# Kernel optimization log

Hardware: AMD Instinct MI355X
Metric: run time of the kernel (lower is better)

Reference implementation:

```python
import jax, jax.numpy as jnp
import numpy as np

N = 40000      # num nodes
E = 640000     # num edges (avg degree 16)
D = 128        # hidden_size
L = 2          # num_gcn


def setup_inputs() -> dict:
    key = jax.random.key(0)
    k1, k2, k3, k4, k5, k6 = jax.random.split(key, 6)
    h = jax.random.normal(k1, (N, D), dtype=jnp.float32)
    edge_src = jax.random.randint(k2, (E,), 0, N, dtype=jnp.int32)
    edge_dst = jax.random.randint(k3, (E,), 0, N, dtype=jnp.int32)
    w_self = jax.random.uniform(k4, (E,), dtype=jnp.float32)
    w_ppi = jax.random.uniform(k5, (E,), dtype=jnp.float32)
    # Xavier-uniform linear weights, zero bias (matches reset_parameters)
    limit = float(np.sqrt(6.0 / (D + D)))
    W = jax.random.uniform(k6, (L, D, D), dtype=jnp.float32, minval=-limit, maxval=limit)
    b = jnp.zeros((L, D), dtype=jnp.float32)
    return {"h": h, "edge_src": edge_src, "edge_dst": edge_dst,
            "w_self": w_self, "w_ppi": w_ppi, "W": W, "b": b}


def _agg(h, src, dst, w):
    # edge-weighted SpMM: sum over incoming edges of w_e * h[src_e]
    msgs = h[src] * w[:, None]                       # [E, D]
    return jax.ops.segment_sum(msgs, dst, num_segments=N)  # [N, D]


def reference(h, edge_src, edge_dst, w_self, w_ppi, W, b):
    for l in range(L):
        res = _agg(h, edge_src, edge_dst, w_self)        # residual aggregation
        ppi = _agg(h, edge_src, edge_dst, w_ppi)         # ppi aggregation
        # NodeUpdate: dropout(relu(linear(ppi))) + res  (dropout=0 -> identity)
        h = jax.nn.relu(ppi @ W[l].T + b[l]) + res
    return h
```

## Files before the change

kernel.cpp:

```cpp
#include <hip/hip_runtime.h>

#define D 128
#define TILE 16
#define CAP 64

typedef short bf16x8 __attribute__((ext_vector_type(8)));
typedef float f32x4  __attribute__((ext_vector_type(4)));
typedef float f32x2  __attribute__((ext_vector_type(2)));

static __device__ __forceinline__ unsigned f2bf(float x) {
    unsigned u = __float_as_uint(x);
    return (u + 0x7FFFu + ((u >> 16) & 1u)) >> 16;
}
static __device__ __forceinline__ float blo(unsigned v) { return __uint_as_float(v << 16); }
static __device__ __forceinline__ float bhi(unsigned v) { return __uint_as_float(v & 0xFFFF0000u); }

__global__ __launch_bounds__(256) void cvt2z_kernel(const float4* __restrict__ a,
                                                    uint2* __restrict__ oa, int n4a,
                                                    const float4* __restrict__ bsrc,
                                                    uint2* __restrict__ ob, int n4b,
                                                    int4* __restrict__ zbuf, int nz4) {
    int i = blockIdx.x * 256 + threadIdx.x;
    if (i < n4a) {
        float4 v = a[i];
        uint2 o;
        o.x = f2bf(v.x) | (f2bf(v.y) << 16);
        o.y = f2bf(v.z) | (f2bf(v.w) << 16);
        oa[i] = o;
    }
    int j = i - n4a;
    if (j >= 0 && j < n4b) {
        float4 v = bsrc[j];
        uint2 o;
        o.x = f2bf(v.x) | (f2bf(v.y) << 16);
        o.y = f2bf(v.z) | (f2bf(v.w) << 16);
        ob[j] = o;
    }
    int k = j - n4b;
    if (k >= 0 && k < nz4) zbuf[k] = make_int4(0, 0, 0, 0);
}

__global__ __launch_bounds__(256) void build_kernel(const int* __restrict__ src,
                                                    const int* __restrict__ dst,
                                                    const float* __restrict__ wself,
                                                    const float* __restrict__ wppi,
                                                    int* __restrict__ cnt,
                                                    uint2* __restrict__ edges, int E) {
    int i = blockIdx.x * 256 + threadIdx.x;
    if (i < E) {
        int d = dst[i];
        int r = atomicAdd(&cnt[d], 1);
        if (r < CAP) {
            uint2 e;
            e.x = (unsigned)src[i];
            e.y = f2bf(wself[i]) | (f2bf(wppi[i]) << 16);
            edges[(d << 6) + r] = e;
        }
    }
}

__global__ __launch_bounds__(512, 6) void layer_kernel(const unsigned short* __restrict__ h16,
                                                       const int* __restrict__ cnt,
                                                       const uint2* __restrict__ edges,
                                                       const unsigned short* __restrict__ Wb,
                                                       const float* __restrict__ bias,
                                                       float* __restrict__ out,
                                                       unsigned short* __restrict__ out16,
                                                       int n) {
    __shared__ unsigned short ppi_lds[TILE][136];
    __shared__ float          res_lds[TILE][132];
    int t = threadIdx.x;
    int w = t >> 6, lane = t & 63;
    int tile = blockIdx.x;
    int q  = lane >> 4;
    int c8 = lane & 15;

    #pragma unroll
    for (int sub = 0; sub < 2; ++sub) {
        int nd   = sub * 8 + w;
        int node = tile * TILE + nd;
        int beg = node << 6;
        int end = beg + cnt[node];
        f32x2 ra[4] = {{0.f,0.f},{0.f,0.f},{0.f,0.f},{0.f,0.f}};
        f32x2 pa[4] = {{0.f,0.f},{0.f,0.f},{0.f,0.f},{0.f,0.f}};
        if (beg < end) {
            int e = beg;
            for (; e + 16 <= end; e += 16) {
                uint2 er[4];
                #pragma unroll
                for (int j = 0; j < 4; ++j) er[j] = edges[e + 4 * j + q];
                uint4 hv[4];
                #pragma unroll
                for (int j = 0; j < 4; ++j)
                    hv[j] = *(const uint4*)(h16 + (size_t)er[j].x * D + c8 * 8);
                #pragma unroll
                for (int j = 0; j < 4; ++j) {
                    float a = blo(er[j].y), b = bhi(er[j].y);
                    f32x2 av = {a, a}, bv = {b, b};
                    f32x2 h01 = {blo(hv[j].x), bhi(hv[j].x)};
                    f32x2 h23 = {blo(hv[j].y), bhi(hv[j].y)};
                    f32x2 h45 = {blo(hv[j].z), bhi(hv[j].z)};
                    f32x2 h67 = {blo(hv[j].w), bhi(hv[j].w)};
                    ra[0] = __builtin_elementwise_fma(av, h01, ra[0]);
                    ra[1] = __builtin_elementwise_fma(av, h23, ra[1]);
                    ra[2] = __builtin_elementwise_fma(av, h45, ra[2]);
                    ra[3] = __builtin_elementwise_fma(av, h67, ra[3]);
                    pa[0] = __builtin_elementwise_fma(bv, h01, pa[0]);
                    pa[1] = __builtin_elementwise_fma(bv, h23, pa[1]);
                    pa[2] = __builtin_elementwise_fma(bv, h45, pa[2]);
                    pa[3] = __builtin_elementwise_fma(bv, h67, pa[3]);
                }
            }
            if (e < end) {
                uint2 er[4];
                float sc[4];
                #pragma unroll
                for (int j = 0; j < 4; ++j) {
                    int idx = e + 4 * j + q;
                    bool act = idx < end;
                    er[j] = edges[act ? idx : beg];
                    sc[j] = act ? 1.f : 0.f;
                }
                uint4 hv[4];
                #pragma unroll
                for (int j = 0; j < 4; ++j)
                    hv[j] = *(const uint4*)(h16 + (size_t)er[j].x * D + c8 * 8);
                #pragma unroll
                for (int j = 0; j < 4; ++j) {
                    float a = blo(er[j].y) * sc[j], b = bhi(er[j].y) * sc[j];
                    f32x2 av = {a, a}, bv = {b, b};
                    f32x2 h01 = {blo(hv[j].x), bhi(hv[j].x)};
                    f32x2 h23 = {blo(hv[j].y), bhi(hv[j].y)};
                    f32x2 h45 = {blo(hv[j].z), bhi(hv[j].z)};
                    f32x2 h67 = {blo(hv[j].w), bhi(hv[j].w)};
                    ra[0] = __builtin_elementwise_fma(av, h01, ra[0]);
                    ra[1] = __builtin_elementwise_fma(av, h23, ra[1]);
                    ra[2] = __builtin_elementwise_fma(av, h45, ra[2]);
                    ra[3] = __builtin_elementwise_fma(av, h67, ra[3]);
                    pa[0] = __builtin_elementwise_fma(bv, h01, pa[0]);
                    pa[1] = __builtin_elementwise_fma(bv, h23, pa[1]);
                    pa[2] = __builtin_elementwise_fma(bv, h45, pa[2]);
                    pa[3] = __builtin_elementwise_fma(bv, h67, pa[3]);
                }
            }
        }
        float r[8] = {ra[0].x, ra[0].y, ra[1].x, ra[1].y, ra[2].x, ra[2].y, ra[3].x, ra[3].y};
        float p[8] = {pa[0].x, pa[0].y, pa[1].x, pa[1].y, pa[2].x, pa[2].y, pa[3].x, pa[3].y};
        #pragma unroll
        for (int i = 0; i < 8; ++i) {
            r[i] += __shfl_xor(r[i], 16, 64);
            r[i] += __shfl_xor(r[i], 32, 64);
            p[i] += __shfl_xor(p[i], 16, 64);
            p[i] += __shfl_xor(p[i], 32, 64);
        }
        if (q == 0) {
            *(float4*)&res_lds[nd][c8 * 8]     = make_float4(r[0], r[1], r[2], r[3]);
            *(float4*)&res_lds[nd][c8 * 8 + 4] = make_float4(r[4], r[5], r[6], r[7]);
            uint4 o;
            o.x = f2bf(p[0]) | (f2bf(p[1]) << 16);
            o.y = f2bf(p[2]) | (f2bf(p[3]) << 16);
            o.z = f2bf(p[4]) | (f2bf(p[5]) << 16);
            o.w = f2bf(p[6]) | (f2bf(p[7]) << 16);
            *(uint4*)&ppi_lds[nd][c8 * 8] = o;
        }
    }
    __syncthreads();

    {
        int m16 = lane & 15, quad = lane >> 4;
        bf16x8 a[4];
        const unsigned short* arow = &ppi_lds[m16][quad * 8];
        #pragma unroll
        for (int kt = 0; kt < 4; ++kt) a[kt] = *(const bf16x8*)(arow + kt * 32);

        const unsigned short* brow = Wb + (size_t)(w * 16 + m16) * D + quad * 8;
        bf16x8 bfr[4];
        #pragma unroll
        for (int kt = 0; kt < 4; ++kt) bfr[kt] = *(const bf16x8*)(brow + kt * 32);

        f32x4 acc = {0.f, 0.f, 0.f, 0.f};
        #pragma unroll
        for (int kt = 0; kt < 4; ++kt)
            acc = __builtin_amdgcn_mfma_f32_16x16x32_bf16(a[kt], bfr[kt], acc, 0, 0, 0);

        int o = w * 16 + m16;
        float bb = bias[o];
        #pragma unroll
        for (int r = 0; r < 4; ++r) {
            int nd = quad * 4 + r;
            float v = fmaxf(acc[r] + bb, 0.f) + res_lds[nd][o];
            size_t gi = (size_t)(tile * TILE + nd) * D + o;
            if (out)   out[gi] = v;
            if (out16) out16[gi] = (unsigned short)f2bf(v);
        }
    }
}

extern "C" void kernel_launch(void* const* d_in, const int* in_sizes, int n_in,
                              void* d_out, int out_size, void* d_ws, size_t ws_size,
                              hipStream_t stream) {
    const float* h0    = (const float*)d_in[0];
    const int*   esrc  = (const int*)d_in[1];
    const int*   edst  = (const int*)d_in[2];
    const float* wself = (const float*)d_in[3];
    const float* wppi  = (const float*)d_in[4];
    const float* W     = (const float*)d_in[5];
    const float* b     = (const float*)d_in[6];
    float*       out   = (float*)d_out;

    const int N = in_sizes[0] / D;
    const int E = in_sizes[1];
    const int L = in_sizes[5] / (D * D);

    char* ws = (char*)d_ws;
    unsigned short* h16a  = (unsigned short*)ws; ws += (size_t)N * D * 2;
    unsigned short* h16b  = (unsigned short*)ws; ws += (size_t)N * D * 2;
    uint2*          edges = (uint2*)ws;          ws += (size_t)N * CAP * 8;
    unsigned short* Wb    = (unsigned short*)ws; ws += (size_t)L * D * D * 2;
    int* cnt = (int*)ws;  ws += (size_t)N * 4;

    int n4h = N * D / 4;
    int n4w = L * D * D / 4;
    int nz4 = N / 4;
    int tot = n4h + n4w + nz4;
    cvt2z_kernel<<<(tot + 255) / 256, 256, 0, stream>>>(
        (const float4*)h0, (uint2*)h16a, n4h,
        (const float4*)W, (uint2*)Wb, n4w,
        (int4*)cnt, nz4);

    int eb = (E + 255) / 256;
    build_kernel<<<eb, 256, 0, stream>>>(esrc, edst, wself, wppi, cnt, edges, E);

    int ntiles = N / TILE;
    layer_kernel<<<ntiles, 512, 0, stream>>>(h16a, cnt, edges, Wb, b,
                                             (L > 1) ? nullptr : out,
                                             (L > 1) ? h16b : nullptr, N);
    for (int l = 1; l < L; ++l) {
        bool last = (l + 1 == L);
        layer_kernel<<<ntiles, 512, 0, stream>>>(h16b, cnt, edges,
                                                 Wb + (size_t)l * D * D, b + (size_t)l * D,
                                                 last ? out : nullptr,
                                                 last ? nullptr : h16a, N);
        unsigned short* tmp = h16a; h16a = h16b; h16b = tmp;
    }
}
```

Baseline: 191.3 us.

## Prefetch edge lists for both nodes and hoist weight loads before aggregation

Loads the first 32 edge records for both nodes of each wave up front, and also the MFMA weight fragments and bias before the gather phase. Each node's first 16 or 32 feature rows are then gathered in one batch, with a loop only for the remaining edges. The aim is more memory-level parallelism and hiding edge-load latency behind feature gathers. In exchange it raises register pressure (launch bounds occupancy hint lowered from 6 to 4) and adds clamping of source indices to the node range.

```diff
diff --git a/kernel.cpp b/kernel.cpp
--- a/kernel.cpp
+++ b/kernel.cpp
@@ -59,7 +59,77 @@
     }
 }
 
-__global__ __launch_bounds__(512, 6) void layer_kernel(const unsigned short* __restrict__ h16,
+static __device__ __forceinline__ void edge_fma(uint2 er, uint4 hv, float sc,
+                                                f32x2 (&ra)[4], f32x2 (&pa)[4]) {
+    float a = blo(er.y) * sc, b = bhi(er.y) * sc;
+    f32x2 av = {a, a}, bv = {b, b};
+    f32x2 h01 = {blo(hv.x), bhi(hv.x)};
+    f32x2 h23 = {blo(hv.y), bhi(hv.y)};
+    f32x2 h45 = {blo(hv.z), bhi(hv.z)};
+    f32x2 h67 = {blo(hv.w), bhi(hv.w)};
+    ra[0] = __builtin_elementwise_fma(av, h01, ra[0]);
+    ra[1] = __builtin_elementwise_fma(av, h23, ra[1]);
+    ra[2] = __builtin_elementwise_fma(av, h45, ra[2]);
+    ra[3] = __builtin_elementwise_fma(av, h67, ra[3]);
+    pa[0] = __builtin_elementwise_fma(bv, h01, pa[0]);
+    pa[1] = __builtin_elementwise_fma(bv, h23, pa[1]);
+    pa[2] = __builtin_elementwise_fma(bv, h45, pa[2]);
+    pa[3] = __builtin_elementwise_fma(bv, h67, pa[3]);
+}
+
+static __device__ __forceinline__ void agg_node(const unsigned short* __restrict__ h16,
+                                                const uint2* __restrict__ edges,
+                                                const uint2 (&er)[8], int cn, int beg,
+                                                int q, int c8, int nn,
+                                                f32x2 (&ra)[4], f32x2 (&pa)[4]) {
+    unsigned s[8]; float sc[8];
+    #pragma unroll
+    for (int j = 0; j < 8; ++j) {
+        int slot = 4 * j + q;
+        bool act = slot < cn;
+        unsigned sj = act ? er[j].x : er[0].x;
+        s[j] = sj < (unsigned)nn ? sj : 0u;
+        sc[j] = act ? 1.f : 0.f;
+    }
+    uint4 hv[8];
+    #pragma unroll
+    for (int j = 0; j < 4; ++j)
+        hv[j] = *(const uint4*)(h16 + (size_t)s[j] * D + c8 * 8);
+    if (cn > 16) {
+        #pragma unroll
+        for (int j = 4; j < 8; ++j)
+            hv[j] = *(const uint4*)(h16 + (size_t)s[j] * D + c8 * 8);
+    }
+    #pragma unroll
+    for (int j = 0; j < 4; ++j) edge_fma(er[j], hv[j], sc[j], ra, pa);
+    if (cn > 16) {
+        #pragma unroll
+        for (int j = 4; j < 8; ++j) edge_fma(er[j], hv[j], sc[j], ra, pa);
+    }
+    if (cn > 32) {
+        int end = beg + cn;
+        for (int e = beg + 32; e < end; e += 16) {
+            uint2 err[4]; float scc[4];
+            #pragma unroll
+            for (int j = 0; j < 4; ++j) {
+                int idx = e + 4 * j + q;
+                bool act = idx < end;
+                err[j] = edges[act ? idx : beg];
+                scc[j] = act ? 1.f : 0.f;
+            }
+            uint4 hh[4];
+            #pragma unroll
+            for (int j = 0; j < 4; ++j) {
+                unsigned sj = err[j].x < (unsigned)nn ? err[j].x : 0u;
+                hh[j] = *(const uint4*)(h16 + (size_t)sj * D + c8 * 8);
+            }
+            #pragma unroll
+            for (int j = 0; j < 4; ++j) edge_fma(err[j], hh[j], scc[j], ra, pa);
+        }
+    }
+}
+
+__global__ __launch_bounds__(512, 4) void layer_kernel(const unsigned short* __restrict__ h16,
                                                        const int* __restrict__ cnt,
                                                        const uint2* __restrict__ edges,
                                                        const unsigned short* __restrict__ Wb,
@@ -75,75 +145,33 @@
     int q  = lane >> 4;
     int c8 = lane & 15;
 
+    int m16 = lane & 15, quad = lane >> 4;
+    bf16x8 bfr[4];
+    const unsigned short* brow = Wb + (size_t)(w * 16 + m16) * D + quad * 8;
+    #pragma unroll
+    for (int kt = 0; kt < 4; ++kt) bfr[kt] = *(const bf16x8*)(brow + kt * 32);
+    float bb = bias[w * 16 + m16];
+
+    int cn[2], beg[2];
+    uint2 er[2][8];
     #pragma unroll
     for (int sub = 0; sub < 2; ++sub) {
-        int nd   = sub * 8 + w;
-        int node = tile * TILE + nd;
-        int beg = node << 6;
-        int end = beg + cnt[node];
+        int node = tile * TILE + sub * 8 + w;
+        beg[sub] = node << 6;
+        cn[sub]  = cnt[node];
+        #pragma unroll
+        for (int j = 0; j < 8; ++j) er[sub][j] = edges[beg[sub] + 4 * j + q];
+    }
+
+    #pragma unroll
+    for (int sub = 0; sub < 2; ++sub) {
+        int nd = sub * 8 + w;
+        int c = cn[sub] < CAP ? cn[sub] : CAP;
         f32x2 ra[4] = {{0.f,0.f},{0.f,0.f},{0.f,0.f},{0.f,0.f}};
         f32x2 pa[4] = {{0.f,0.f},{0.f,0.f},{0.f,0.f},{0.f,0.f}};
-        if (beg < end) {
-            int e = beg;
-            for (; e + 16 <= end; e += 16) {
-                uint2 er[4];
-                #pragma unroll
-                for (int j = 0; j < 4; ++j) er[j] = edges[e + 4 * j + q];
-                uint4 hv[4];
-                #pragma unroll
-                for (int j = 0; j < 4; ++j)
-                    hv[j] = *(const uint4*)(h16 + (size_t)er[j].x * D + c8 * 8);
-                #pragma unroll
-                for (int j = 0; j < 4; ++j) {
-                    float a = blo(er[j].y), b = bhi(er[j].y);
-                    f32x2 av = {a, a}, bv = {b, b};
-                    f32x2 h01 = {blo(hv[j].x), bhi(hv[j].x)};
-                    f32x2 h23 = {blo(hv[j].y), bhi(hv[j].y)};
-                    f32x2 h45 = {blo(hv[j].z), bhi(hv[j].z)};
-                    f32x2 h67 = {blo(hv[j].w), bhi(hv[j].w)};
-                    ra[0] = __builtin_elementwise_fma(av, h01, ra[0]);
-                    ra[1] = __builtin_elementwise_fma(av, h23, ra[1]);
-                    ra[2] = __builtin_elementwise_fma(av, h45, ra[2]);
-                    ra[3] = __builtin_elementwise_fma(av, h67, ra[3]);
-                    pa[0] = __builtin_elementwise_fma(bv, h01, pa[0]);
-                    pa[1] = __builtin_elementwise_fma(bv, h23, pa[1]);
-                    pa[2] = __builtin_elementwise_fma(bv, h45, pa[2]);
-                    pa[3] = __builtin_elementwise_fma(bv, h67, pa[3]);
-                }
-            }
-            if (e < end) {
-                uint2 er[4];
-                float sc[4];
-                #pragma unroll
-                for (int j = 0; j < 4; ++j) {
-                    int idx = e + 4 * j + q;
-                    bool act = idx < end;
-                    er[j] = edges[act ? idx : beg];
-                    sc[j] = act ? 1.f : 0.f;
-                }
-                uint4 hv[4];
-                #pragma unroll
-                for (int j = 0; j < 4; ++j)
-                    hv[j] = *(const uint4*)(h16 + (size_t)er[j].x * D + c8 * 8);
-                #pragma unroll
-                for (int j = 0; j < 4; ++j) {
-                    float a = blo(er[j].y) * sc[j], b = bhi(er[j].y) * sc[j];
-                    f32x2 av = {a, a}, bv = {b, b};
-                    f32x2 h01 = {blo(hv[j].x), bhi(hv[j].x)};
-                    f32x2 h23 = {blo(hv[j].y), bhi(hv[j].y)};
-                    f32x2 h45 = {blo(hv[j].z), bhi(hv[j].z)};
-                    f32x2 h67 = {blo(hv[j].w), bhi(hv[j].w)};
-                    ra[0] = __builtin_elementwise_fma(av, h01, ra[0]);
-                    ra[1] = __builtin_elementwise_fma(av, h23, ra[1]);
-                    ra[2] = __builtin_elementwise_fma(av, h45, ra[2]);
-                    ra[3] = __builtin_elementwise_fma(av, h67, ra[3]);
-                    pa[0] = __builtin_elementwise_fma(bv, h01, pa[0]);
-                    pa[1] = __builtin_elementwise_fma(bv, h23, pa[1]);
-                    pa[2] = __builtin_elementwise_fma(bv, h45, pa[2]);
-                    pa[3] = __builtin_elementwise_fma(bv, h67, pa[3]);
-                }
-            }
-        }
+        if (c > 0)
+            agg_node(h16, edges, er[sub], c, beg[sub], q, c8, n, ra, pa);
+
         float r[8] = {ra[0].x, ra[0].y, ra[1].x, ra[1].y, ra[2].x, ra[2].y, ra[3].x, ra[3].y};
         float p[8] = {pa[0].x, pa[0].y, pa[1].x, pa[1].y, pa[2].x, pa[2].y, pa[3].x, pa[3].y};
         #pragma unroll
@@ -167,24 +195,17 @@
     __syncthreads();
 
     {
-        int m16 = lane & 15, quad = lane >> 4;
         bf16x8 a[4];
         const unsigned short* arow = &ppi_lds[m16][quad * 8];
         #pragma unroll
         for (int kt = 0; kt < 4; ++kt) a[kt] = *(const bf16x8*)(arow + kt * 32);
 
-        const unsigned short* brow = Wb + (size_t)(w * 16 + m16) * D + quad * 8;
-        bf16x8 bfr[4];
-        #pragma unroll
-        for (int kt = 0; kt < 4; ++kt) bfr[kt] = *(const bf16x8*)(brow + kt * 32);
-
         f32x4 acc = {0.f, 0.f, 0.f, 0.f};
         #pragma unroll
         for (int kt = 0; kt < 4; ++kt)
             acc = __builtin_amdgcn_mfma_f32_16x16x32_bf16(a[kt], bfr[kt], acc, 0, 0, 0);
 
         int o = w * 16 + m16;
-        float bb = bias[o];
         #pragma unroll
         for (int r = 0; r < 4; ++r) {
             int nd = quad * 4 + r;
```

Result: no change. 193.1 us (+1.0%).
